# Performance work log

Measured on AMD Instinct MI355X. Metric: run time of the kernel, lower is better.

Reference implementation:

```python
import jax, jax.numpy as jnp
import numpy as np

HEADS = 4
HEAD_DIM = 128  # GATConv out_channels
NEG_SLOPE_ATT = 0.2   # GATConv internal leaky relu
NEG_SLOPE_ACT = 0.01  # nn.LeakyReLU() default


def gat_conv(x, edge_index, W, att_src, att_dst, bias):
    # x: [N, F]; edge_index: [2, E] (row 0 = src j, row 1 = dst i)
    N = x.shape[0]
    h = (x @ W).reshape(N, HEADS, HEAD_DIM)            # [N, H, C]
    loops = jnp.arange(N, dtype=edge_index.dtype)
    src = jnp.concatenate([edge_index[0], loops])      # add self loops
    dst = jnp.concatenate([edge_index[1], loops])
    a_src = jnp.einsum('nhc,hc->nh', h, att_src)       # [N, H]
    a_dst = jnp.einsum('nhc,hc->nh', h, att_dst)
    e = jax.nn.leaky_relu(a_src[src] + a_dst[dst], NEG_SLOPE_ATT)  # [E', H]
    # segment softmax over incoming edges of each dst node
    emax = jax.ops.segment_max(e, dst, num_segments=N)
    ex = jnp.exp(e - emax[dst])
    denom = jax.ops.segment_sum(ex, dst, num_segments=N)
    alpha = ex / (denom[dst] + 1e-16)                  # [E', H]
    msg = h[src] * alpha[:, :, None]                   # [E', H, C]
    out = jax.ops.segment_sum(msg, dst, num_segments=N)
    return out.reshape(N, HEADS * HEAD_DIM) + bias     # [N, H*C]


def branch(x, edge_index, W, att_src, att_dst, bias, fc1_w, fc1_b):
    h = gat_conv(x, edge_index, W, att_src, att_dst, bias)
    h = jax.nn.leaky_relu(h, NEG_SLOPE_ACT)
    g = jnp.mean(h, axis=0, keepdims=True)             # global mean pool, batch all zeros -> [1, H*C]
    g = jax.nn.leaky_relu(g @ fc1_w + fc1_b, NEG_SLOPE_ACT)
    return g  # dropout is identity in eval mode


def setup_inputs() -> dict:
    key = jax.random.key(0)
    ks = jax.random.split(key, 10)
    N, E, F = 20000, 320000, 512
    HC = HEADS * HEAD_DIM
    s = 1.0 / np.sqrt(F)
    return {
        'x': jax.random.normal(ks[0], (N, F), jnp.float32),
        'adj': jax.random.randint(ks[1], (2, E), 0, N, jnp.int64),
        'wt_x': jax.random.normal(ks[2], (N, F), jnp.float32),
        'wt_adj': jax.random.randint(ks[3], (2, E), 0, N, jnp.int64),
        'W': jax.random.normal(ks[4], (F, HC), jnp.float32) * s,
        'att_src': jax.random.normal(ks[5], (HEADS, HEAD_DIM), jnp.float32) * s,
        'att_dst': jax.random.normal(ks[6], (HEADS, HEAD_DIM), jnp.float32) * s,
        'bias': jnp.zeros((HC,), jnp.float32),
        'fc1_w': jax.random.normal(ks[7], (HC, 512), jnp.float32) * (1.0 / np.sqrt(HC)),
        'fc1_b': jnp.zeros((512,), jnp.float32),
    }


def reference(x, adj, wt_x, wt_adj, W, att_src, att_dst, bias, fc1_w, fc1_b):
    g = branch(x, adj, W, att_src, att_dst, bias, fc1_w, fc1_b)
    wt_g = branch(wt_x, wt_adj, W, att_src, att_dst, bias, fc1_w, fc1_b)
    xd = g - wt_g
    return jnp.concatenate([g, wt_g, xd], axis=1)  # [1, 3*512]
```

## Files before the change

### kernel.cpp

```cpp
#include <hip/hip_runtime.h>
#include <hip/hip_bf16.h>

typedef unsigned short u16;
typedef short bf16x8 __attribute__((ext_vector_type(8)));
typedef float f32x4 __attribute__((ext_vector_type(4)));
typedef float f32x2 __attribute__((ext_vector_type(2)));

__device__ __forceinline__ u16 f2b(float f) {
    unsigned x = __float_as_uint(f);
    return (u16)((x + 0x7fffu + ((x >> 16) & 1u)) >> 16);
}

__device__ __forceinline__ int pkbf(float lo, float hi) {
    return __builtin_amdgcn_perm(__float_as_uint(hi), __float_as_uint(lo), 0x07060302);
}

__device__ __forceinline__ void pkfma(f32x2& acc, f32x2 f, f32x2 ex) {
    asm("v_pk_fma_f32 %0, %1, %2, %0" : "+v"(acc) : "v"(f), "v"(ex));
}

__global__ __launch_bounds__(256) void cast_wt_kernel(const float* __restrict__ W,
                                                      u16* __restrict__ Wt) {
    __shared__ u16 tile[64][65];
    int tx = threadIdx.x & 63, ty = threadIdx.x >> 6;
    int bx = blockIdx.x & 7, by = blockIdx.x >> 3;
#pragma unroll
    for (int r = 0; r < 16; ++r) {
        int row = ty + (r << 2);
        tile[tx][row] = f2b(W[(by * 64 + row) * 512 + bx * 64 + tx]);
    }
    __syncthreads();
#pragma unroll
    for (int r = 0; r < 16; ++r) {
        int row = ty + (r << 2);
        Wt[(bx * 64 + row) * 512 + by * 64 + tx] = tile[row][tx];
    }
}

__global__ __launch_bounds__(256, 2) void gemm_fused5(
    const float* __restrict__ xA, const float* __restrict__ xW, const u16* __restrict__ Bt,
    unsigned char* __restrict__ h8, const float* __restrict__ att_src,
    const float* __restrict__ att_dst, float* __restrict__ asrc, float* __restrict__ adst,
    int N, int Mpad) {
    __shared__ float lA[64 * 32];
    __shared__ u16 lB[512 * 32];
    const int tid = threadIdx.x;
    const int w = tid >> 6, l = tid & 63;
    const int row0 = blockIdx.x * 64;
    const int head = w;
    const int mlane = l & 15, quad = l >> 4;
    const int R2v = 2 * Mpad;

    const float* src = (row0 >= Mpad) ? xW : xA;
    const int rbase = row0 - (row0 >= Mpad ? Mpad : 0);
    const int arow = (l >> 3);
    const int acol = (((l & 7) ^ arow) << 2);
    const int brow = (l >> 2);
    const int bcol = (((l & 3) ^ ((l >> 3) & 3)) << 3);

    f32x4 acc[4][8];
#pragma unroll
    for (int i = 0; i < 4; i++)
#pragma unroll
        for (int j = 0; j < 8; j++) acc[i][j] = f32x4{0.f, 0.f, 0.f, 0.f};

    for (int k0 = 0; k0 < 512; k0 += 32) {
#pragma unroll
        for (int g = 0; g < 2; ++g) {
            int lrow = rbase + (w << 4) + (g << 3) + arow;
            lrow = min(lrow, N - 1);
            const float* ga = src + (size_t)lrow * 512 + k0 + acol;
            float* la = lA + (((w << 4) + (g << 3)) << 5);
            __builtin_amdgcn_global_load_lds((const __attribute__((address_space(1))) void*)ga,
                                             (__attribute__((address_space(3))) void*)la, 16, 0, 0);
        }
#pragma unroll
        for (int s = 0; s < 8; ++s) {
            const u16* gb = Bt + (size_t)((w << 7) + (s << 4) + brow) * 512 + (k0 + bcol);
            u16* lb = lB + (((w << 7) + (s << 4)) << 5);
            __builtin_amdgcn_global_load_lds((const __attribute__((address_space(1))) void*)gb,
                                             (__attribute__((address_space(3))) void*)lb, 16, 0, 0);
        }
        __syncthreads();
        bf16x8 af[4], bfr[8];
#pragma unroll
        for (int i = 0; i < 4; i++) {
            const float* rb = &lA[(i * 16 + mlane) * 32];
            float4 f0 = *(const float4*)(rb + (((quad * 2) ^ (mlane & 7)) << 2));
            float4 f1 = *(const float4*)(rb + (((quad * 2 + 1) ^ (mlane & 7)) << 2));
            int* ai = (int*)&af[i];
            ai[0] = pkbf(f0.x, f0.y);
            ai[1] = pkbf(f0.z, f0.w);
            ai[2] = pkbf(f1.x, f1.y);
            ai[3] = pkbf(f1.z, f1.w);
        }
#pragma unroll
        for (int j = 0; j < 8; j++)
            bfr[j] = *(const bf16x8*)&lB[((w << 7) + j * 16 + mlane) * 32 +
                                         ((quad ^ ((mlane >> 1) & 3)) << 3)];
#pragma unroll
        for (int i = 0; i < 4; i++)
#pragma unroll
            for (int j = 0; j < 8; j++)
                acc[i][j] = __builtin_amdgcn_mfma_f32_16x16x32_bf16(af[i], bfr[j], acc[i][j], 0, 0, 0);
        __syncthreads();
    }

    float as_j[8], ad_j[8];
#pragma unroll
    for (int j = 0; j < 8; j++) {
        as_j[j] = att_src[(head << 7) + j * 16 + mlane];
        ad_j[j] = att_dst[(head << 7) + j * 16 + mlane];
    }
#pragma unroll
    for (int i = 0; i < 4; i++) {
#pragma unroll
        for (int r = 0; r < 4; r++) {
            float vs = 0.f, vd = 0.f;
#pragma unroll
            for (int j = 0; j < 8; j++) {
                float hv = acc[i][j][r];
                vs += hv * as_j[j];
                vd += hv * ad_j[j];
            }
#pragma unroll
            for (int o = 8; o >= 1; o >>= 1) {
                vs += __shfl_xor(vs, o);
                vd += __shfl_xor(vd, o);
            }
            if (mlane == 0) {
                int rg = row0 + i * 16 + quad * 4 + r;
                asrc[head * R2v + rg] = vs;
                adst[head * R2v + rg] = vd;
            }
        }
    }
#pragma unroll
    for (int i = 0; i < 4; i++)
#pragma unroll
        for (int j = 0; j < 8; j++)
#pragma unroll
            for (int r = 0; r < 4; r++) {
                int rg = row0 + i * 16 + quad * 4 + r;
                int cc = j * 16 + mlane;
                float v = acc[i][j][r];
                unsigned pk = __builtin_amdgcn_cvt_pk_fp8_f32(v, v, 0, false);
                h8[(((size_t)(head * R2v + rg)) << 7) + cc] = (unsigned char)(pk & 0xff);
            }
}

__global__ void csr_count(const int* __restrict__ adj, const int* __restrict__ wadj,
                          int E, int Mpad, int* __restrict__ deg) {
    int i = blockIdx.x * blockDim.x + threadIdx.x;
    if (i < 2 * E) {
        int d = (i < E) ? adj[E + i] : (wadj[E + (i - E)] + Mpad);
        atomicAdd(&deg[d], 1);
    }
}

__global__ __launch_bounds__(256) void scanA(const int* __restrict__ deg, int* __restrict__ off,
                                             int* __restrict__ bsum, int n, int N, int Mpad) {
    __shared__ int wsum[4];
    int tid = threadIdx.x, lane = tid & 63, wid = tid >> 6;
    int i = blockIdx.x * 256 + tid;
    int valid = (i < N) || (i >= Mpad && i < Mpad + N);
    int d = (i < n) ? deg[i] + (valid ? 1 : 0) : 0;
    int x = d;
#pragma unroll
    for (int o = 1; o < 64; o <<= 1) {
        int y = __shfl_up(x, (unsigned)o, 64);
        if (lane >= o) x += y;
    }
    if (lane == 63) wsum[wid] = x;
    __syncthreads();
    int woff = 0;
    for (int j = 0; j < wid; ++j) woff += wsum[j];
    if (i < n) off[i] = woff + x - d;
    if (tid == 255) bsum[blockIdx.x] = woff + x;
}

__global__ __launch_bounds__(256) void scanB(const int* __restrict__ bsum, int* __restrict__ bbase,
                                             int nb, int* __restrict__ off, int n) {
    __shared__ int wsum[4];
    int tid = threadIdx.x, lane = tid & 63, wid = tid >> 6;
    int d = (tid < nb) ? bsum[tid] : 0;
    int x = d;
#pragma unroll
    for (int o = 1; o < 64; o <<= 1) {
        int y = __shfl_up(x, (unsigned)o, 64);
        if (lane >= o) x += y;
    }
    if (lane == 63) wsum[wid] = x;
    __syncthreads();
    int woff = 0;
    for (int j = 0; j < wid; ++j) woff += wsum[j];
    int excl = woff + x - d;
    if (tid < nb) bbase[tid] = excl;
    if (tid == nb - 1) off[n] = excl + d;
}

__global__ void scanC(int* __restrict__ off, const int* __restrict__ bbase,
                      int* __restrict__ cursor, int* __restrict__ csrc, int n, int N, int Mpad) {
    int i = blockIdx.x * blockDim.x + threadIdx.x;
    if (i < n) {
        int o = off[i] + bbase[i >> 8];
        off[i] = o;
        int valid = (i < N) || (i >= Mpad && i < Mpad + N);
        if (valid) csrc[o] = i;
        cursor[i] = o + valid;
    }
}

__global__ void csr_scatter(const int* __restrict__ adj, const int* __restrict__ wadj,
                            int E, int Mpad, int* __restrict__ cursor, int* __restrict__ csrc) {
    int i = blockIdx.x * blockDim.x + threadIdx.x;
    if (i < 2 * E) {
        int s, d;
        if (i < E) {
            s = adj[i];
            d = adj[E + i];
        } else {
            s = wadj[i - E] + Mpad;
            d = wadj[E + (i - E)] + Mpad;
        }
        int p = atomicAdd(&cursor[d], 1);
        csrc[p] = s;
    }
}

__global__ __launch_bounds__(256, 6) void gat_aggregate13(
    const unsigned char* __restrict__ h8, const float* __restrict__ asrc,
    const float* __restrict__ adst, const int* __restrict__ off, const int* __restrict__ csrc,
    const float* __restrict__ bias, float* __restrict__ partAB, int Mpad) {
    const int R2 = 2 * Mpad;
    __shared__ float spool[128];
    int tid = threadIdx.x;
    if (tid < 128) spool[tid] = 0.f;
    __syncthreads();
    const int wv = tid >> 6, l = tid & 63;
    const int gi = (l >> 3) & 3;
    const int hi = l >> 5;
    const int chb = (l & 7) << 4;
    const int head = (blockIdx.x & 7) >> 1;
    const int gc = blockIdx.x & 1;
    const unsigned char* h8h = h8 + (((size_t)head * R2) << 7);
    const float* ash = asrc + (size_t)head * R2;
    const float* adh = adst + (size_t)head * R2;
    float bb[16];
#pragma unroll
    for (int k = 0; k < 16; ++k) bb[k] = bias[head * 128 + chb + k];
    float pool[16];
#pragma unroll
    for (int k = 0; k < 16; ++k) pool[k] = 0.f;

    const int hb = gc * Mpad;
    const int half = Mpad >> 1;
    int widx = ((blockIdx.x >> 3) << 2) + wv;
    const int cstride = gridDim.x >> 1;

    for (int p = widx; p < half; p += cstride) {
        int d0 = (p << 1) + hb;
        int q0 = off[d0], q1 = off[d0 + 1], q2 = off[d0 + 2];
        int n0 = q1 - q0, n1 = q2 - q1;
        int nmax = max(n0, n1);
        if (nmax == 0) continue;
        int nm = hi ? n1 : n0;
        int qm = hi ? q1 : q0;
        float ad = adh[d0 + hi];
        f32x2 acc2[8];
#pragma unroll
        for (int j = 0; j < 8; ++j) acc2[j] = f32x2{0.f, 0.f};
        float dsum = 0.f;

        int i0 = gi, i1 = 4 + gi, i2 = 8 + gi, i3 = 12 + gi;
        int E0 = csrc[qm + ((i0 < nm) ? i0 : 0)];
        int E1 = csrc[qm + ((i1 < nm) ? i1 : 0)];
        int E2 = csrc[qm + ((i2 < nm) ? i2 : 0)];
        int E3 = csrc[qm + ((i3 < nm) ? i3 : 0)];
        float A0 = ash[E0];
        int4 H0 = *(const int4*)(h8h + (((size_t)E0) << 7) + chb);
        float A1 = ash[E1];
        int4 H1 = *(const int4*)(h8h + (((size_t)E1) << 7) + chb);

#pragma unroll 2
        for (int base = 0; base < nmax; base += 4) {
            int i4 = base + 16 + gi;
            int E4 = csrc[qm + ((i4 < nm) ? i4 : 0)];
            float A2 = ash[E2];
            int4 H2 = *(const int4*)(h8h + (((size_t)E2) << 7) + chb);
            float e = A0 + ad;
            float em = fmaxf(e, 0.2f * e);
            float ex = __expf(em);
            ex = ((base + gi) < nm) ? ex : 0.f;
            dsum += ex;
            f32x2 exv = {ex, ex};
            f32x2 f;
            f = __builtin_amdgcn_cvt_pk_f32_fp8(H0.x, false); pkfma(acc2[0], f, exv);
            f = __builtin_amdgcn_cvt_pk_f32_fp8(H0.x, true);  pkfma(acc2[1], f, exv);
            f = __builtin_amdgcn_cvt_pk_f32_fp8(H0.y, false); pkfma(acc2[2], f, exv);
            f = __builtin_amdgcn_cvt_pk_f32_fp8(H0.y, true);  pkfma(acc2[3], f, exv);
            f = __builtin_amdgcn_cvt_pk_f32_fp8(H0.z, false); pkfma(acc2[4], f, exv);
            f = __builtin_amdgcn_cvt_pk_f32_fp8(H0.z, true);  pkfma(acc2[5], f, exv);
            f = __builtin_amdgcn_cvt_pk_f32_fp8(H0.w, false); pkfma(acc2[6], f, exv);
            f = __builtin_amdgcn_cvt_pk_f32_fp8(H0.w, true);  pkfma(acc2[7], f, exv);
            A0 = A1; H0 = H1;
            A1 = A2; H1 = H2;
            E2 = E3; E3 = E4;
        }
        dsum += __shfl_xor(dsum, 8);
        dsum += __shfl_xor(dsum, 16);
#pragma unroll
        for (int j = 0; j < 8; ++j) {
            acc2[j].x += __shfl_xor(acc2[j].x, 8);
            acc2[j].y += __shfl_xor(acc2[j].y, 8);
            acc2[j].x += __shfl_xor(acc2[j].x, 16);
            acc2[j].y += __shfl_xor(acc2[j].y, 16);
        }
        if (nm > 0) {
            float inv = 1.f / (dsum + 1e-16f);
#pragma unroll
            for (int j = 0; j < 8; ++j) {
                float o0 = acc2[j].x * inv + bb[2 * j];
                float o1 = acc2[j].y * inv + bb[2 * j + 1];
                pool[2 * j] += fmaxf(o0, 0.01f * o0);
                pool[2 * j + 1] += fmaxf(o1, 0.01f * o1);
            }
        }
    }
    if ((l & 31) < 8) {
#pragma unroll
        for (int k = 0; k < 16; ++k) atomicAdd(&spool[chb + k], pool[k]);
    }
    __syncthreads();
    if (tid < 128) {
        int slot = (blockIdx.x >> 3) & 63;
        float* dp = partAB + (gc ? 64 * 512 : 0) + (slot << 9) + head * 128 + tid;
        atomicAdd(dp, spool[tid]);
    }
}

__global__ __launch_bounds__(256) void fc_final2(
    const float* __restrict__ partAB, const float* __restrict__ w, const float* __restrict__ b,
    float* __restrict__ out, float invN) {
    __shared__ float gA[512], gB[512];
    __shared__ float rA[256], rB[256];
    int t = threadIdx.x;
    for (int i = t; i < 512; i += 256) {
        float sA = 0.f, sB = 0.f;
        for (int r = 0; r < 64; ++r) {
            sA += partAB[r * 512 + i];
            sB += partAB[64 * 512 + r * 512 + i];
        }
        gA[i] = sA * invN;
        gB[i] = sB * invN;
    }
    __syncthreads();
    int jj = t & 31, ks = t >> 5;
    int j = blockIdx.x * 32 + jj;
    float sA = 0.f, sB = 0.f;
    for (int k = ks * 64; k < ks * 64 + 64; ++k) {
        float wv = w[k * 512 + j];
        sA += gA[k] * wv;
        sB += gB[k] * wv;
    }
    rA[t] = sA;
    rB[t] = sB;
    __syncthreads();
    if (ks == 0) {
#pragma unroll
        for (int s2 = 1; s2 < 8; ++s2) {
            sA += rA[jj + 32 * s2];
            sB += rB[jj + 32 * s2];
        }
        sA += b[j];
        sB += b[j];
        sA = sA >= 0.f ? sA : 0.01f * sA;
        sB = sB >= 0.f ? sB : 0.01f * sB;
        out[j] = sA;
        out[512 + j] = sB;
        out[1024 + j] = sA - sB;
    }
}

extern "C" void kernel_launch(void* const* d_in, const int* in_sizes, int n_in,
                              void* d_out, int out_size, void* d_ws, size_t ws_size,
                              hipStream_t stream) {
    const float* x = (const float*)d_in[0];
    const int* adj = (const int*)d_in[1];
    const float* wtx = (const float*)d_in[2];
    const int* wadj = (const int*)d_in[3];
    const float* W = (const float*)d_in[4];
    const float* att_s = (const float*)d_in[5];
    const float* att_d = (const float*)d_in[6];
    const float* bias = (const float*)d_in[7];
    const float* fc1w = (const float*)d_in[8];
    const float* fc1b = (const float*)d_in[9];
    float* out = (float*)d_out;

    const int N = in_sizes[0] / 512;
    const int E = in_sizes[1] / 2;
    const int Mpad = ((N + 127) / 128) * 128;
    const int R2 = 2 * Mpad;
    const int nb = (R2 + 255) / 256;

    char* p = (char*)d_ws;
    auto alloc = [&](size_t bytes) -> char* {
        char* r = p;
        p += (bytes + 255) & ~(size_t)255;
        return r;
    };
    unsigned char* h8 = (unsigned char*)alloc((size_t)R2 * 512);
    u16* Wt = (u16*)alloc(512 * 512 * 2);
    float* asrc = (float*)alloc((size_t)R2 * 4 * 4);
    float* adst = (float*)alloc((size_t)R2 * 4 * 4);
    int* deg = (int*)alloc((size_t)R2 * 4);
    int* off = (int*)alloc((size_t)(R2 + 1) * 4);
    int* cursor = (int*)alloc((size_t)R2 * 4);
    int* bsum = (int*)alloc(256 * 4);
    int* bbase = (int*)alloc(256 * 4);
    int* csrc = (int*)alloc((size_t)2 * (E + N) * 4);
    float* partAB = (float*)alloc((size_t)2 * 64 * 512 * 4);

    hipMemsetAsync(partAB, 0, (size_t)2 * 64 * 512 * 4, stream);
    hipMemsetAsync(deg, 0, (size_t)R2 * 4, stream);
    cast_wt_kernel<<<64, 256, 0, stream>>>(W, Wt);

    csr_count<<<(2 * E + 255) / 256, 256, 0, stream>>>(adj, wadj, E, Mpad, deg);
    scanA<<<nb, 256, 0, stream>>>(deg, off, bsum, R2, N, Mpad);
    scanB<<<1, 256, 0, stream>>>(bsum, bbase, nb, off, R2);
    scanC<<<nb, 256, 0, stream>>>(off, bbase, cursor, csrc, R2, N, Mpad);
    csr_scatter<<<(2 * E + 255) / 256, 256, 0, stream>>>(adj, wadj, E, Mpad, cursor, csrc);

    gemm_fused5<<<R2 / 64, 256, 0, stream>>>(x, wtx, Wt, h8, att_s, att_d, asrc, adst, N, Mpad);

    gat_aggregate13<<<1536, 256, 0, stream>>>(h8, asrc, adst, off, csrc, bias, partAB, Mpad);

    fc_final2<<<16, 256, 0, stream>>>(partAB, fc1w, fc1b, out, 1.0f / (float)N);
}
```

Baseline: 331.3 us.

## Double-buffer GEMM LDS tiles and stage fp8 output through LDS for coalesced stores

The GEMM kernel now double-buffers its A and B shared-memory tiles, so the global-to-LDS load of the next K slice is issued before the MFMAs on the current slice, and one barrier per iteration is dropped. The fp8 epilogue used to write single bytes scattered straight to global memory. It now writes them into a swizzled LDS staging buffer and then stores coalesced 16-byte chunks. The trade-off is that LDS use roughly doubles (about 80KB per block), which may lower occupancy below the two blocks per CU requested in the launch bounds.

Measured after the change: 326.6 us. Within noise of the previous version (-1.4%).

```diff
diff --git a/kernel.cpp b/kernel.cpp
--- a/kernel.cpp
+++ b/kernel.cpp
@@ -37,13 +37,13 @@
     }
 }
 
-__global__ __launch_bounds__(256, 2) void gemm_fused5(
+__global__ __launch_bounds__(256, 2) void gemm_fused6(
     const float* __restrict__ xA, const float* __restrict__ xW, const u16* __restrict__ Bt,
     unsigned char* __restrict__ h8, const float* __restrict__ att_src,
     const float* __restrict__ att_dst, float* __restrict__ asrc, float* __restrict__ adst,
     int N, int Mpad) {
-    __shared__ float lA[64 * 32];
-    __shared__ u16 lB[512 * 32];
+    __shared__ float lA[2][64 * 32];
+    __shared__ u16 lB[2][512 * 32];
     const int tid = threadIdx.x;
     const int w = tid >> 6, l = tid & 63;
     const int row0 = blockIdx.x * 64;
@@ -58,34 +58,40 @@
     const int brow = (l >> 2);
     const int bcol = (((l & 3) ^ ((l >> 3) & 3)) << 3);
 
-    f32x4 acc[4][8];
-#pragma unroll
-    for (int i = 0; i < 4; i++)
-#pragma unroll
-        for (int j = 0; j < 8; j++) acc[i][j] = f32x4{0.f, 0.f, 0.f, 0.f};
-
-    for (int k0 = 0; k0 < 512; k0 += 32) {
+    auto stage = [&](int b, int k0) {
 #pragma unroll
         for (int g = 0; g < 2; ++g) {
             int lrow = rbase + (w << 4) + (g << 3) + arow;
             lrow = min(lrow, N - 1);
             const float* ga = src + (size_t)lrow * 512 + k0 + acol;
-            float* la = lA + (((w << 4) + (g << 3)) << 5);
+            float* la = &lA[b][((w << 4) + (g << 3)) << 5];
             __builtin_amdgcn_global_load_lds((const __attribute__((address_space(1))) void*)ga,
                                              (__attribute__((address_space(3))) void*)la, 16, 0, 0);
         }
 #pragma unroll
         for (int s = 0; s < 8; ++s) {
             const u16* gb = Bt + (size_t)((w << 7) + (s << 4) + brow) * 512 + (k0 + bcol);
-            u16* lb = lB + (((w << 7) + (s << 4)) << 5);
+            u16* lb = &lB[b][((w << 7) + (s << 4)) << 5];
             __builtin_amdgcn_global_load_lds((const __attribute__((address_space(1))) void*)gb,
                                              (__attribute__((address_space(3))) void*)lb, 16, 0, 0);
         }
-        __syncthreads();
+    };
+
+    f32x4 acc[4][8];
+#pragma unroll
+    for (int i = 0; i < 4; i++)
+#pragma unroll
+        for (int j = 0; j < 8; j++) acc[i][j] = f32x4{0.f, 0.f, 0.f, 0.f};
+
+    stage(0, 0);
+    __syncthreads();
+    int cur = 0;
+    for (int t = 0; t < 16; ++t) {
+        if (t < 15) stage(cur ^ 1, (t + 1) << 5);
         bf16x8 af[4], bfr[8];
 #pragma unroll
         for (int i = 0; i < 4; i++) {
-            const float* rb = &lA[(i * 16 + mlane) * 32];
+            const float* rb = &lA[cur][(i * 16 + mlane) * 32];
             float4 f0 = *(const float4*)(rb + (((quad * 2) ^ (mlane & 7)) << 2));
             float4 f1 = *(const float4*)(rb + (((quad * 2 + 1) ^ (mlane & 7)) << 2));
             int* ai = (int*)&af[i];
@@ -96,14 +102,15 @@
         }
 #pragma unroll
         for (int j = 0; j < 8; j++)
-            bfr[j] = *(const bf16x8*)&lB[((w << 7) + j * 16 + mlane) * 32 +
-                                         ((quad ^ ((mlane >> 1) & 3)) << 3)];
+            bfr[j] = *(const bf16x8*)&lB[cur][((w << 7) + j * 16 + mlane) * 32 +
+                                             ((quad ^ ((mlane >> 1) & 3)) << 3)];
 #pragma unroll
         for (int i = 0; i < 4; i++)
 #pragma unroll
             for (int j = 0; j < 8; j++)
                 acc[i][j] = __builtin_amdgcn_mfma_f32_16x16x32_bf16(af[i], bfr[j], acc[i][j], 0, 0, 0);
         __syncthreads();
+        cur ^= 1;
     }
 
     float as_j[8], ad_j[8];
@@ -135,18 +142,32 @@
             }
         }
     }
+
+    unsigned char* hstage = (unsigned char*)&lB[0][0];
 #pragma unroll
     for (int i = 0; i < 4; i++)
 #pragma unroll
         for (int j = 0; j < 8; j++)
 #pragma unroll
             for (int r = 0; r < 4; r++) {
-                int rg = row0 + i * 16 + quad * 4 + r;
-                int cc = j * 16 + mlane;
+                int row = i * 16 + quad * 4 + r;
+                int colb = (w << 7) + j * 16 + mlane;
                 float v = acc[i][j][r];
                 unsigned pk = __builtin_amdgcn_cvt_pk_fp8_f32(v, v, 0, false);
-                h8[(((size_t)(head * R2v + rg)) << 7) + cc] = (unsigned char)(pk & 0xff);
+                hstage[row * 512 + (colb ^ ((row & 7) << 4))] = (unsigned char)(pk & 0xff);
             }
+    __syncthreads();
+#pragma unroll
+    for (int k = 0; k < 8; ++k) {
+        int c = (k << 8) + tid;
+        int hd = c >> 9;
+        int rem = c & 511;
+        int row = rem >> 3;
+        int cch = rem & 7;
+        int lofs = row * 512 + ((((hd << 7) + (cch << 4))) ^ ((row & 7) << 4));
+        int4 v = *(const int4*)&hstage[lofs];
+        *(int4*)&h8[(((size_t)(hd * R2v + row0 + row)) << 7) + (cch << 4)] = v;
+    }
 }
 
 __global__ void csr_count(const int* __restrict__ adj, const int* __restrict__ wadj,
@@ -431,7 +452,7 @@
     scanC<<<nb, 256, 0, stream>>>(off, bbase, cursor, csrc, R2, N, Mpad);
     csr_scatter<<<(2 * E + 255) / 256, 256, 0, stream>>>(adj, wadj, E, Mpad, cursor, csrc);
 
-    gemm_fused5<<<R2 / 64, 256, 0, stream>>>(x, wtx, Wt, h8, att_s, att_d, asrc, adst, N, Mpad);
+    gemm_fused6<<<R2 / 64, 256, 0, stream>>>(x, wtx, Wt, h8, att_s, att_d, asrc, adst, N, Mpad);
 
     gat_aggregate13<<<1536, 256, 0, stream>>>(h8, asrc, adst, off, csrc, bias, partAB, Mpad);
 
```
